# Optimization experiments

Hardware: AMD Instinct MI355X
Metric: run time of the kernel (lower is better)

Reference implementation:

```python
import jax, jax.numpy as jnp
import numpy as np

B, T, D = 16384, 3, 512   # batch, task_num, input_dim
G = T + 1                  # expert groups (idx 0 shared)
NE = 4                     # experts per group
H, E = 512, 256            # expert hidden, expert output dim (layers=[512,256])
GH = 256                   # gate hidden
TH, TO = 128, 64           # tower hidden / output dims


def setup_inputs() -> dict:
    key = jax.random.key(0)
    ks = jax.random.split(key, 14)
    s = 0.02
    return {
        "inputs": jax.random.normal(ks[0], (B, G, D), jnp.float32),
        # expert MLPs: [group, expert, ...]
        "expert_W1": jax.random.normal(ks[1], (G, NE, D, H), jnp.float32) * s,
        "expert_b1": jnp.zeros((G, NE, H), jnp.float32),
        "expert_W2": jax.random.normal(ks[2], (G, NE, H, E), jnp.float32) * s,
        "expert_b2": jnp.zeros((G, NE, E), jnp.float32),
        # per-task gates (softmax over G*NE experts)
        "gate_W1": jax.random.normal(ks[3], (T, D, GH), jnp.float32) * s,
        "gate_b1": jnp.zeros((T, GH), jnp.float32),
        "gate_W2": jax.random.normal(ks[4], (T, GH, G * NE), jnp.float32) * s,
        "gate_b2": jnp.zeros((T, G * NE), jnp.float32),
        # per-task towers (is_last=True)
        "tower_W1": jax.random.normal(ks[5], (T, E, TH), jnp.float32) * s,
        "tower_b1": jnp.zeros((T, TH), jnp.float32),
        "tower_W2": jax.random.normal(ks[6], (T, TH, TO), jnp.float32) * s,
        "tower_b2": jnp.zeros((T, TO), jnp.float32),
    }


def reference(inputs, expert_W1, expert_b1, expert_W2, expert_b2,
              gate_W1, gate_b1, gate_W2, gate_b2,
              tower_W1, tower_b1, tower_W2, tower_b2):
    b = inputs.shape[0]
    g, ne = expert_W1.shape[0], expert_W1.shape[1]
    t_num = gate_W1.shape[0]

    # All expert groups in one batched einsum: [B, G, NE, E]
    h1 = jax.nn.relu(jnp.einsum('bgd,gndh->bgnh', inputs, expert_W1) + expert_b1)
    emb = jnp.einsum('bgnh,gnhe->bgne', h1, expert_W2) + expert_b2

    # Task gates on (task input + shared input): softmax over G*NE experts
    gin = inputs[:, 1:, :] + inputs[:, :1, :]                      # [B, T, D]
    gh = jax.nn.relu(jnp.einsum('btd,tdh->bth', gin, gate_W1) + gate_b1)
    gw = jax.nn.softmax(jnp.einsum('bth,thk->btk', gh, gate_W2) + gate_b2, axis=-1)  # [B,T,G*NE]

    emb_sg = jax.lax.stop_gradient(emb)
    group_ids = jnp.arange(g)
    outs = []
    for t in range(t_num):
        # gradient flows only through shared group (0) and own group (t+1)
        keep = (group_ids == 0) | (group_ids == t + 1)              # [G]
        masked = jnp.where(keep[None, :, None, None], emb, emb_sg)  # [B,G,NE,E]
        agg = jnp.einsum('bk,bke->be', gw[:, t], masked.reshape(b, g * ne, -1))  # [B,E]
        th = jax.nn.relu(agg @ tower_W1[t] + tower_b1[t])
        outs.append(th @ tower_W2[t] + tower_b2[t])                 # [B,TO]
    return jnp.concatenate(outs, axis=1)                           # [B, T*TO]
```

## Files before the change

kernel.cpp:

```cpp
#include <hip/hip_runtime.h>
#include <math.h>

#define B_N  16384
#define T_N  3
#define D_N  512
#define G_N  4
#define NE_N 4
#define H_N  512
#define E_N  256
#define GH_N 256
#define K16  16
#define TH_N 128
#define TO_N 64

typedef __attribute__((ext_vector_type(8))) short short8;
typedef __attribute__((ext_vector_type(4))) float floatx4;

__device__ __forceinline__ unsigned short f2bf(float f) {
    union { float f; unsigned u; } v; v.f = f;
    unsigned r = (v.u + 0x7fffu + ((v.u >> 16) & 1u)) >> 16;
    return (unsigned short)r;
}
__device__ __forceinline__ float bf2f(unsigned short h) {
    union { unsigned u; float f; } v; v.u = ((unsigned)h) << 16;
    return v.f;
}
__device__ __forceinline__ unsigned pack2(float lo, float hi) {
    return ((unsigned)f2bf(hi) << 16) | (unsigned)f2bf(lo);
}

typedef const __attribute__((address_space(1))) void gvoid_t;
typedef __attribute__((address_space(3))) void lvoid_t;

#if __has_builtin(__builtin_amdgcn_global_load_lds)
#define HAVE_GLL 1
__device__ __forceinline__ void load_lds16(const void* g, void* l) {
    __builtin_amdgcn_global_load_lds((gvoid_t*)g, (lvoid_t*)l, 16, 0, 0);
}
#else
#define HAVE_GLL 0
#endif

__global__ __launch_bounds__(256) void convert_inputs(
    const float* __restrict__ x, unsigned short* __restrict__ xb,
    unsigned short* __restrict__ ginb)
{
    const long b = blockIdx.x;
    const int tid = threadIdx.x;
    const float* xr = x + b * (G_N * D_N);
    unsigned short* xo = xb + b * (G_N * D_N);
    unsigned short* go = ginb + b * (T_N * D_N);
    float2 v0 = *(const float2*)&xr[tid * 2];
    *(unsigned*)&xo[tid * 2] = pack2(v0.x, v0.y);
    #pragma unroll
    for (int g = 1; g < G_N; ++g) {
        float2 v = *(const float2*)&xr[g * D_N + tid * 2];
        *(unsigned*)&xo[g * D_N + tid * 2] = pack2(v.x, v.y);
        *(unsigned*)&go[(g - 1) * D_N + tid * 2] = pack2(v.x + v0.x, v.y + v0.y);
    }
}

__global__ __launch_bounds__(256) void prep_kernel(
    const float* __restrict__ eW1, const float* __restrict__ eW2,
    const float* __restrict__ gW1, const float* __restrict__ tW1,
    const float* __restrict__ tW2,
    unsigned short* __restrict__ W1t, unsigned short* __restrict__ W2t,
    unsigned short* __restrict__ G1t, unsigned short* __restrict__ TW1t,
    unsigned short* __restrict__ TW2t,
    const float* __restrict__ x, unsigned short* __restrict__ xb,
    unsigned short* __restrict__ ginb)
{
    const int bid = blockIdx.x;
    if (bid < 6648) {
        const float* in; unsigned short* out; int K, N, nx, local;
        if (bid < 4096)      { in = eW1; out = W1t;  K = 512; N = 512; nx = 16; local = bid; }
        else if (bid < 6144) { in = eW2; out = W2t;  K = 512; N = 256; nx = 8;  local = bid - 4096; }
        else if (bid < 6528) { in = gW1; out = G1t;  K = 512; N = 256; nx = 8;  local = bid - 6144; }
        else if (bid < 6624) { in = tW1; out = TW1t; K = 256; N = 128; nx = 4;  local = bid - 6528; }
        else                 { in = tW2; out = TW2t; K = 128; N = 64;  nx = 2;  local = bid - 6624; }
        const int ny = K / 32;
        const int xt = local % nx;
        const int yt = (local / nx) % ny;
        const int z  = local / (nx * ny);
        __shared__ float tile[32][33];
        const int tx = threadIdx.x & 31, ty = threadIdx.x >> 5;
        const long zo = (long)z * K * N;
        const int n0 = xt * 32, k0 = yt * 32;
        #pragma unroll
        for (int i = 0; i < 4; ++i)
            tile[ty + 8 * i][tx] = in[zo + (long)(k0 + ty + 8 * i) * N + n0 + tx];
        __syncthreads();
        #pragma unroll
        for (int i = 0; i < 4; ++i)
            out[zo + (long)(n0 + ty + 8 * i) * K + k0 + tx] = f2bf(tile[tx][ty + 8 * i]);
    } else {
        const long b = bid - 6648;
        const int tid = threadIdx.x;
        const float* xr = x + b * (G_N * D_N);
        unsigned short* xo = xb + b * (G_N * D_N);
        unsigned short* go = ginb + b * (T_N * D_N);
        float2 v0 = *(const float2*)&xr[tid * 2];
        *(unsigned*)&xo[tid * 2] = pack2(v0.x, v0.y);
        #pragma unroll
        for (int g = 1; g < G_N; ++g) {
            float2 v = *(const float2*)&xr[g * D_N + tid * 2];
            *(unsigned*)&xo[g * D_N + tid * 2] = pack2(v.x, v.y);
            *(unsigned*)&go[(g - 1) * D_N + tid * 2] = pack2(v.x + v0.x, v.y + v0.y);
        }
    }
}

template<int RELU>
__global__ __launch_bounds__(256) void gemm_bf16(
    const unsigned short* __restrict__ A, int lda, int a_zoff,
    const unsigned short* __restrict__ Bt, int bt_zoff,
    const float* __restrict__ bias, int bias_zoff,
    unsigned short* __restrict__ C, int ldc, int c_zoff, int K)
{
    __shared__ __align__(16) unsigned short As[2][128 * 32];
    __shared__ __align__(16) unsigned short Bs[2][128 * 32];
    const int tid = threadIdx.x;
    const int z = blockIdx.z;
    const long m0 = (long)blockIdx.x * 128;
    const long n0 = (long)blockIdx.y * 128;
    const unsigned short* Ab = A + (long)z * a_zoff + m0 * lda;
    const unsigned short* Bb = Bt + (long)z * bt_zoff + n0 * K;
    const int lane16 = tid & 15;
    const int quad = (tid & 63) >> 4;
    const int wave = tid >> 6;
    const int wm = (wave >> 1) * 64;
    const int wn = (wave & 1) * 64;
    const int srow = tid >> 2;
    const int scolsw = (((tid & 3) ^ ((tid >> 3) & 3)) * 8);
    const int cw8 = ((quad ^ ((lane16 >> 1) & 3)) * 8);

    floatx4 acc[4][4] = {};

    for (int k0 = 0; k0 < K; k0 += 64) {
        #pragma unroll
        for (int h = 0; h < 2; ++h) {
            const int kh = k0 + h * 32;
#if HAVE_GLL
            load_lds16(Ab + (long)srow * lda + kh + scolsw, &As[h][tid * 8]);
            load_lds16(Ab + (long)(srow + 64) * lda + kh + scolsw, &As[h][2048 + tid * 8]);
            load_lds16(Bb + (long)srow * K + kh + scolsw, &Bs[h][tid * 8]);
            load_lds16(Bb + (long)(srow + 64) * K + kh + scolsw, &Bs[h][2048 + tid * 8]);
#else
            *(uint4*)&As[h][tid * 8] = *(const uint4*)(Ab + (long)srow * lda + kh + scolsw);
            *(uint4*)&As[h][2048 + tid * 8] = *(const uint4*)(Ab + (long)(srow + 64) * lda + kh + scolsw);
            *(uint4*)&Bs[h][tid * 8] = *(const uint4*)(Bb + (long)srow * K + kh + scolsw);
            *(uint4*)&Bs[h][2048 + tid * 8] = *(const uint4*)(Bb + (long)(srow + 64) * K + kh + scolsw);
#endif
        }
        __syncthreads();
        #pragma unroll
        for (int h = 0; h < 2; ++h) {
            short8 a[4], b[4];
            #pragma unroll
            for (int mi = 0; mi < 4; ++mi)
                a[mi] = *(const short8*)&As[h][(wm + mi * 16 + lane16) * 32 + cw8];
            #pragma unroll
            for (int ni = 0; ni < 4; ++ni)
                b[ni] = *(const short8*)&Bs[h][(wn + ni * 16 + lane16) * 32 + cw8];
            #pragma unroll
            for (int mi = 0; mi < 4; ++mi)
                #pragma unroll
                for (int ni = 0; ni < 4; ++ni)
                    acc[mi][ni] = __builtin_amdgcn_mfma_f32_16x16x32_bf16(
                        a[mi], b[ni], acc[mi][ni], 0, 0, 0);
        }
        __syncthreads();
    }

    unsigned short* Cb = C + (long)z * c_zoff + m0 * ldc + n0;
    const float* bb = bias + (long)z * bias_zoff + n0;
    #pragma unroll
    for (int mi = 0; mi < 4; ++mi) {
        #pragma unroll
        for (int ni = 0; ni < 4; ++ni) {
            const int col = wn + ni * 16 + lane16;
            const float bv = bb[col];
            #pragma unroll
            for (int r = 0; r < 4; ++r) {
                const int row = wm + mi * 16 + quad * 4 + r;
                float v = acc[mi][ni][r] + bv;
                if (RELU) v = fmaxf(v, 0.0f);
                Cb[(long)row * ldc + col] = f2bf(v);
            }
        }
    }
}

__global__ __launch_bounds__(256, 2) void expert_fused(
    const unsigned short* __restrict__ xb,
    const unsigned short* __restrict__ W1t,
    const float* __restrict__ eb1,
    const unsigned short* __restrict__ W2t,
    const float* __restrict__ eb2,
    unsigned short* __restrict__ embb)
{
    __shared__ __align__(16) unsigned short sm[33792];
    unsigned short* As  = sm;
    unsigned short* Bs  = sm + 8192;
    unsigned short* h1s = sm + 16384;

    const int tid = threadIdx.x;
    const unsigned bid = blockIdx.x;
    const int e = ((bid & 7) << 1) | ((bid >> 3) & 1);
    const long m0 = (long)(bid >> 4) * 128;
    const int g = e >> 2;

    const unsigned short* Ab  = xb + m0 * 2048 + g * 512;
    const unsigned short* W1b = W1t + (long)e * (512 * 512);
    const unsigned short* W2b = W2t + (long)e * (256 * 512);

    const int lane16 = tid & 15;
    const int quad = (tid & 63) >> 4;
    const int wave = tid >> 6;
    const int wm  = (wave >> 1) * 64;
    const int wn  = (wave & 1) * 64;
    const int wn2 = (wave & 1) * 128;
    const int srow = tid >> 2;
    const int scolsw = (((tid & 3) ^ ((tid >> 3) & 3)) * 8);
    const int cw8 = ((quad ^ ((lane16 >> 1) & 3)) * 8);

    floatx4 acc2[4][8] = {};

    for (int nc = 0; nc < 4; ++nc) {
        const unsigned short* Bb = W1b + ((long)nc << 16);
        floatx4 acc[4][4] = {};
        for (int k0 = 0; k0 < 512; k0 += 64) {
            #pragma unroll
            for (int h = 0; h < 2; ++h) {
                const int kh = k0 + h * 32;
#if HAVE_GLL
                load_lds16(Ab + (long)srow * 2048 + kh + scolsw, &As[h * 4096 + tid * 8]);
                load_lds16(Ab + (long)(srow + 64) * 2048 + kh + scolsw, &As[h * 4096 + 2048 + tid * 8]);
                load_lds16(Bb + (long)srow * 512 + kh + scolsw, &Bs[h * 4096 + tid * 8]);
                load_lds16(Bb + (long)(srow + 64) * 512 + kh + scolsw, &Bs[h * 4096 + 2048 + tid * 8]);
#else
                *(uint4*)&As[h * 4096 + tid * 8] = *(const uint4*)(Ab + (long)srow * 2048 + kh + scolsw);
                *(uint4*)&As[h * 4096 + 2048 + tid * 8] = *(const uint4*)(Ab + (long)(srow + 64) * 2048 + kh + scolsw);
                *(uint4*)&Bs[h * 4096 + tid * 8] = *(const uint4*)(Bb + (long)srow * 512 + kh + scolsw);
                *(uint4*)&Bs[h * 4096 + 2048 + tid * 8] = *(const uint4*)(Bb + (long)(srow + 64) * 512 + kh + scolsw);
#endif
            }
            __syncthreads();
            #pragma unroll
            for (int h = 0; h < 2; ++h) {
                short8 b[4];
                #pragma unroll
                for (int ni = 0; ni < 4; ++ni)
                    b[ni] = *(const short8*)&Bs[h * 4096 + (wn + ni * 16 + lane16) * 32 + cw8];
                #pragma unroll
                for (int mi = 0; mi < 4; ++mi) {
                    short8 a = *(const short8*)&As[h * 4096 + (wm + mi * 16 + lane16) * 32 + cw8];
                    #pragma unroll
                    for (int ni = 0; ni < 4; ++ni)
                        acc[mi][ni] = __builtin_amdgcn_mfma_f32_16x16x32_bf16(
                            a, b[ni], acc[mi][ni], 0, 0, 0);
                }
            }
            __syncthreads();
        }
        #pragma unroll
        for (int mi = 0; mi < 4; ++mi) {
            #pragma unroll
            for (int ni = 0; ni < 4; ++ni) {
                const int col = wn + ni * 16 + lane16;
                const float bv = eb1[e * 512 + nc * 128 + col];
                #pragma unroll
                for (int r = 0; r < 4; ++r) {
                    const int row = wm + mi * 16 + quad * 4 + r;
                    h1s[row * 136 + col] = f2bf(fmaxf(acc[mi][ni][r] + bv, 0.0f));
                }
            }
        }
        __syncthreads();
        #pragma unroll
        for (int ks = 0; ks < 128; ks += 32) {
            #pragma unroll
            for (int i = 0; i < 4; ++i) {
#if HAVE_GLL
                load_lds16(W2b + (long)(srow + 64 * i) * 512 + nc * 128 + ks + scolsw,
                           &As[i * 2048 + tid * 8]);
#else
                *(uint4*)&As[i * 2048 + tid * 8] =
                    *(const uint4*)(W2b + (long)(srow + 64 * i) * 512 + nc * 128 + ks + scolsw);
#endif
            }
            __syncthreads();
            #pragma unroll
            for (int nh = 0; nh < 2; ++nh) {
                short8 b2[4];
                #pragma unroll
                for (int nj = 0; nj < 4; ++nj)
                    b2[nj] = *(const short8*)&As[(wn2 + nh * 64 + nj * 16 + lane16) * 32 + cw8];
                #pragma unroll
                for (int mi = 0; mi < 4; ++mi) {
                    short8 a2 = *(const short8*)&h1s[(wm + mi * 16 + lane16) * 136 + ks + quad * 8];
                    #pragma unroll
                    for (int nj = 0; nj < 4; ++nj)
                        acc2[mi][nh * 4 + nj] = __builtin_amdgcn_mfma_f32_16x16x32_bf16(
                            a2, b2[nj], acc2[mi][nh * 4 + nj], 0, 0, 0);
                }
            }
            __syncthreads();
        }
    }

    unsigned short* Cb = embb + m0 * 4096 + (long)e * 256;
    #pragma unroll
    for (int mi = 0; mi < 4; ++mi) {
        #pragma unroll
        for (int j = 0; j < 8; ++j) {
            const int col = wn2 + (j >> 2) * 64 + (j & 3) * 16 + lane16;
            const float bv = eb2[e * 256 + col];
            #pragma unroll
            for (int r = 0; r < 4; ++r) {
                const int row = wm + mi * 16 + quad * 4 + r;
                Cb[(long)row * 4096 + col] = f2bf(acc2[mi][j][r] + bv);
            }
        }
    }
}

__global__ __launch_bounds__(256) void gate2_softmax(
    const unsigned short* __restrict__ gh, const float* __restrict__ W2,
    const float* __restrict__ b2, float* __restrict__ gw)
{
    const int t = blockIdx.y;
    const long b0 = (long)blockIdx.x * 64;
    const int tid = threadIdx.x;
    __shared__ __align__(16) unsigned short ghs[64 * 256];
    __shared__ float ls[64 * 16];
    #pragma unroll
    for (int it = 0; it < 8; ++it) {
        int seg = it * 256 + tid;
        int row = seg >> 5;
        int col = (seg & 31) * 8;
        *(uint4*)&ghs[seg * 8] =
            *(const uint4*)&gh[(b0 + row) * (T_N * GH_N) + (long)t * GH_N + col];
    }
    __syncthreads();
    const float* W2t = W2 + (long)t * GH_N * K16;
    #pragma unroll
    for (int it = 0; it < 4; ++it) {
        int o = it * 256 + tid;
        int b = o >> 4, k = o & 15;
        float acc = b2[t * K16 + k];
        #pragma unroll 8
        for (int h = 0; h < GH_N; ++h)
            acc += bf2f(ghs[b * 256 + h]) * W2t[h * K16 + k];
        ls[o] = acc;
    }
    __syncthreads();
    if (tid < 64) {
        float m = -1e30f;
        #pragma unroll
        for (int k = 0; k < 16; ++k) m = fmaxf(m, ls[tid * 16 + k]);
        float e[16], s = 0.f;
        #pragma unroll
        for (int k = 0; k < 16; ++k) { e[k] = expf(ls[tid * 16 + k] - m); s += e[k]; }
        const float inv = 1.0f / s;
        float* gwp = gw + (b0 + tid) * (T_N * K16) + (long)t * K16;
        #pragma unroll
        for (int k = 0; k < 16; ++k) gwp[k] = e[k] * inv;
    }
}

__global__ __launch_bounds__(256) void agg_kernel(
    const unsigned short* __restrict__ emb, const float* __restrict__ gw,
    unsigned short* __restrict__ aggb, long bc)
{
    const long b = (long)blockIdx.x * 8 + (threadIdx.x >> 5);
    const int e0 = (threadIdx.x & 31) * 8;
    const unsigned short* er = emb + b * 4096 + e0;
    const float* gwr = gw + b * 48;
    float a0[8] = {}, a1[8] = {}, a2[8] = {};
    #pragma unroll
    for (int k = 0; k < 16; ++k) {
        short8 v = *(const short8*)(er + (long)k * 256);
        const float w0 = gwr[k], w1 = gwr[16 + k], w2 = gwr[32 + k];
        #pragma unroll
        for (int j = 0; j < 8; ++j) {
            float f = bf2f((unsigned short)v[j]);
            a0[j] += w0 * f; a1[j] += w1 * f; a2[j] += w2 * f;
        }
    }
    unsigned r0[4] = {pack2(a0[0], a0[1]), pack2(a0[2], a0[3]),
                      pack2(a0[4], a0[5]), pack2(a0[6], a0[7])};
    unsigned r1[4] = {pack2(a1[0], a1[1]), pack2(a1[2], a1[3]),
                      pack2(a1[4], a1[5]), pack2(a1[6], a1[7])};
    unsigned r2[4] = {pack2(a2[0], a2[1]), pack2(a2[2], a2[3]),
                      pack2(a2[4], a2[5]), pack2(a2[6], a2[7])};
    *(uint4*)(aggb + 0L * bc * 256 + b * 256 + e0) = *(uint4*)r0;
    *(uint4*)(aggb + 1L * bc * 256 + b * 256 + e0) = *(uint4*)r1;
    *(uint4*)(aggb + 2L * bc * 256 + b * 256 + e0) = *(uint4*)r2;
}

__global__ __launch_bounds__(256) void tower_fused(
    const unsigned short* __restrict__ aggb, long bc,
    const unsigned short* __restrict__ w1t, const float* __restrict__ tb1,
    const unsigned short* __restrict__ w2t, const float* __restrict__ tb2,
    float* __restrict__ out)
{
    __shared__ __align__(16) unsigned short sm[26112];
    unsigned short* As  = sm;
    unsigned short* Bs  = sm + 4096;
    unsigned short* th  = sm;
    unsigned short* w2s = sm + 17408;
    const int tid = threadIdx.x;
    const int t = blockIdx.y;
    const long m0 = (long)blockIdx.x * 128;
    const unsigned short* Ab = aggb + (long)t * bc * 256 + m0 * 256;
    const unsigned short* Bb = w1t + (long)t * (TH_N * E_N);
    const int lane16 = tid & 15;
    const int quad = (tid & 63) >> 4;
    const int wave = tid >> 6;
    const int wm = (wave >> 1) * 64;
    const int wn = (wave & 1) * 64;
    const int srow = tid >> 2;
    const int scolsw = (((tid & 3) ^ ((tid >> 3) & 3)) * 8);
    const int cw8 = ((quad ^ ((lane16 >> 1) & 3)) * 8);

    #pragma unroll
    for (int i = 0; i < 4; ++i) {
        const int seg = i * 256 + tid;
        const int row = seg >> 4, cb = (seg & 15) * 8;
        *(uint4*)&w2s[row * 136 + cb] =
            *(const uint4*)&w2t[(long)t * (TO_N * TH_N) + (long)row * 128 + cb];
    }

    floatx4 acc[4][4] = {};
    for (int k0 = 0; k0 < 256; k0 += 32) {
#if HAVE_GLL
        load_lds16(Ab + (long)srow * 256 + k0 + scolsw, &As[tid * 8]);
        load_lds16(Ab + (long)(srow + 64) * 256 + k0 + scolsw, &As[2048 + tid * 8]);
        load_lds16(Bb + (long)srow * 256 + k0 + scolsw, &Bs[tid * 8]);
        load_lds16(Bb + (long)(srow + 64) * 256 + k0 + scolsw, &Bs[2048 + tid * 8]);
#else
        *(uint4*)&As[tid * 8] = *(const uint4*)(Ab + (long)srow * 256 + k0 + scolsw);
        *(uint4*)&As[2048 + tid * 8] = *(const uint4*)(Ab + (long)(srow + 64) * 256 + k0 + scolsw);
        *(uint4*)&Bs[tid * 8] = *(const uint4*)(Bb + (long)srow * 256 + k0 + scolsw);
        *(uint4*)&Bs[2048 + tid * 8] = *(const uint4*)(Bb + (long)(srow + 64) * 256 + k0 + scolsw);
#endif
        __syncthreads();
        short8 a[4], b[4];
        #pragma unroll
        for (int mi = 0; mi < 4; ++mi)
            a[mi] = *(const short8*)&As[(wm + mi * 16 + lane16) * 32 + cw8];
        #pragma unroll
        for (int ni = 0; ni < 4; ++ni)
            b[ni] = *(const short8*)&Bs[(wn + ni * 16 + lane16) * 32 + cw8];
        #pragma unroll
        for (int mi = 0; mi < 4; ++mi)
            #pragma unroll
            for (int ni = 0; ni < 4; ++ni)
                acc[mi][ni] = __builtin_amdgcn_mfma_f32_16x16x32_bf16(
                    a[mi], b[ni], acc[mi][ni], 0, 0, 0);
        __syncthreads();
    }

    #pragma unroll
    for (int mi = 0; mi < 4; ++mi) {
        #pragma unroll
        for (int ni = 0; ni < 4; ++ni) {
            const int col = wn + ni * 16 + lane16;
            const float bv = tb1[t * TH_N + col];
            #pragma unroll
            for (int r = 0; r < 4; ++r) {
                const int row = wm + mi * 16 + quad * 4 + r;
                th[row * 136 + col] = f2bf(fmaxf(acc[mi][ni][r] + bv, 0.0f));
            }
        }
    }
    __syncthreads();

    floatx4 acc2[2][4] = {};
    #pragma unroll
    for (int kk = 0; kk < 4; ++kk) {
        short8 a2[2], b2[4];
        #pragma unroll
        for (int mi = 0; mi < 2; ++mi)
            a2[mi] = *(const short8*)&th[(wave * 32 + mi * 16 + lane16) * 136 + kk * 32 + quad * 8];
        #pragma unroll
        for (int ni = 0; ni < 4; ++ni)
            b2[ni] = *(const short8*)&w2s[(ni * 16 + lane16) * 136 + kk * 32 + quad * 8];
        #pragma unroll
        for (int mi = 0; mi < 2; ++mi)
            #pragma unroll
            for (int ni = 0; ni < 4; ++ni)
                acc2[mi][ni] = __builtin_amdgcn_mfma_f32_16x16x32_bf16(
                    a2[mi], b2[ni], acc2[mi][ni], 0, 0, 0);
    }
    #pragma unroll
    for (int mi = 0; mi < 2; ++mi) {
        #pragma unroll
        for (int ni = 0; ni < 4; ++ni) {
            const int col = ni * 16 + lane16;
            const float bv = tb2[t * TO_N + col];
            #pragma unroll
            for (int r = 0; r < 4; ++r) {
                const int row = wave * 32 + mi * 16 + quad * 4 + r;
                out[(m0 + row) * (T_N * TO_N) + t * TO_N + col] = acc2[mi][ni][r] + bv;
            }
        }
    }
}

extern "C" void kernel_launch(void* const* d_in, const int* in_sizes, int n_in,
                              void* d_out, int out_size, void* d_ws, size_t ws_size,
                              hipStream_t stream)
{
    const float* x   = (const float*)d_in[0];
    const float* eW1 = (const float*)d_in[1];
    const float* eb1 = (const float*)d_in[2];
    const float* eW2 = (const float*)d_in[3];
    const float* eb2 = (const float*)d_in[4];
    const float* gW1 = (const float*)d_in[5];
    const float* gb1 = (const float*)d_in[6];
    const float* gW2 = (const float*)d_in[7];
    const float* gb2 = (const float*)d_in[8];
    const float* tW1 = (const float*)d_in[9];
    const float* tb1 = (const float*)d_in[10];
    const float* tW2 = (const float*)d_in[11];
    const float* tb2 = (const float*)d_in[12];
    float* out = (float*)d_out;

    char* ws = (char*)d_ws;
    unsigned short* W1t  = (unsigned short*)(ws + 0);
    unsigned short* W2t  = (unsigned short*)(ws + 8388608);
    unsigned short* G1t  = (unsigned short*)(ws + 12582912);
    unsigned short* TW1t = (unsigned short*)(ws + 13369344);
    unsigned short* TW2t = (unsigned short*)(ws + 13565952);
    const size_t WFIX = 13615104;

    long BCo = 0;
    for (long co = 16384; co >= 128; co >>= 1)
        if (WFIX + (size_t)co * 18624 <= ws_size) { BCo = co; break; }
    if (BCo == 0) return;

    char* p = ws + WFIX;
    unsigned short* xb   = (unsigned short*)p; p += BCo * 4096;
    unsigned short* ginb = (unsigned short*)p; p += BCo * 3072;
    unsigned short* embb = (unsigned short*)p; p += BCo * 8192;
    unsigned short* gh   = (unsigned short*)p; p += BCo * 1536;
    float*          gw   = (float*)p;          p += BCo * 192;
    unsigned short* aggb = (unsigned short*)p;

    const long n_o = B_N / BCo;

    const long nconv = (n_o == 1) ? BCo : 0;
    prep_kernel<<<dim3((unsigned)(6648 + nconv)), 256, 0, stream>>>(
        eW1, eW2, gW1, tW1, tW2, W1t, W2t, G1t, TW1t, TW2t, x, xb, ginb);

    for (long c = 0; c < n_o; ++c) {
        const float* xc = x + c * BCo * (G_N * D_N);
        float* outc = out + c * BCo * (T_N * TO_N);

        if (n_o > 1)
            convert_inputs<<<BCo, 256, 0, stream>>>(xc, xb, ginb);
        gemm_bf16<1><<<dim3(BCo / 128, 2, 3), 256, 0, stream>>>(
            ginb, 1536, 512, G1t, 131072, gb1, 256, gh, 768, 256, 512);
        gate2_softmax<<<dim3(BCo / 64, 3), 256, 0, stream>>>(gh, gW2, gb2, gw);
        expert_fused<<<dim3((BCo / 128) * 16), 256, 0, stream>>>(
            xb, W1t, eb1, W2t, eb2, embb);
        agg_kernel<<<BCo / 8, 256, 0, stream>>>(embb, gw, aggb, BCo);
        tower_fused<<<dim3(BCo / 128, 3), 256, 0, stream>>>(
            aggb, BCo, TW1t, tb1, TW2t, tb2, outc);
    }
}
```

Baseline: 593.1 us.

## Fuse gate GEMM, second gate layer and softmax into one MFMA kernel

Replaces the generic gate hidden-layer GEMM plus the scalar gate2_softmax kernel with a single gate_fused kernel. The 128x256 ReLU hidden tile stays in swizzled LDS, and the second gate layer runs on MFMA with bf16-converted weights. Softmax is done with cross-lane shuffles, which removes the gh round-trip through global memory, one launch, and the scalar FMA loop. In exchange the kernel drops double-buffered K staging, has fewer blocks (one per 128 rows per task), and rounds W2 to bf16.

Result: faster. 563.0 us (median of 2 runs) (-5.1%).

```diff
diff --git a/kernel.cpp b/kernel.cpp
--- a/kernel.cpp
+++ b/kernel.cpp
@@ -110,83 +110,118 @@
     }
 }
 
-template<int RELU>
-__global__ __launch_bounds__(256) void gemm_bf16(
-    const unsigned short* __restrict__ A, int lda, int a_zoff,
-    const unsigned short* __restrict__ Bt, int bt_zoff,
-    const float* __restrict__ bias, int bias_zoff,
-    unsigned short* __restrict__ C, int ldc, int c_zoff, int K)
-{
-    __shared__ __align__(16) unsigned short As[2][128 * 32];
-    __shared__ __align__(16) unsigned short Bs[2][128 * 32];
+__global__ __launch_bounds__(256) void gate_fused(
+    const unsigned short* __restrict__ ginb,
+    const unsigned short* __restrict__ G1t,
+    const float* __restrict__ gb1,
+    const float* __restrict__ gW2,
+    const float* __restrict__ gb2,
+    float* __restrict__ gw)
+{
+    __shared__ __align__(16) unsigned short sm[40960];
+    unsigned short* As  = sm;
+    unsigned short* Bs  = sm + 4096;
+    unsigned short* w2s = sm;
+    unsigned short* ghs = sm + 8192;
+
     const int tid = threadIdx.x;
-    const int z = blockIdx.z;
-    const long m0 = (long)blockIdx.x * 128;
-    const long n0 = (long)blockIdx.y * 128;
-    const unsigned short* Ab = A + (long)z * a_zoff + m0 * lda;
-    const unsigned short* Bb = Bt + (long)z * bt_zoff + n0 * K;
+    const int t = blockIdx.y;
+    const long b0 = (long)blockIdx.x * 128;
+    const unsigned short* Ab = ginb + b0 * 1536 + (long)t * 512;
+
     const int lane16 = tid & 15;
     const int quad = (tid & 63) >> 4;
     const int wave = tid >> 6;
     const int wm = (wave >> 1) * 64;
     const int wn = (wave & 1) * 64;
     const int srow = tid >> 2;
-    const int scolsw = (((tid & 3) ^ ((tid >> 3) & 3)) * 8);
+    const int scol = (((tid & 3) ^ ((tid >> 3) & 3)) * 8);
     const int cw8 = ((quad ^ ((lane16 >> 1) & 3)) * 8);
 
-    floatx4 acc[4][4] = {};
-
-    for (int k0 = 0; k0 < K; k0 += 64) {
-        #pragma unroll
-        for (int h = 0; h < 2; ++h) {
-            const int kh = k0 + h * 32;
+    #pragma unroll
+    for (int ncc = 0; ncc < 2; ++ncc) {
+        const unsigned short* Bb = G1t + (long)t * 131072 + (long)(ncc * 128) * 512;
+        floatx4 acc[4][4] = {};
+        for (int k0 = 0; k0 < 512; k0 += 32) {
 #if HAVE_GLL
-            load_lds16(Ab + (long)srow * lda + kh + scolsw, &As[h][tid * 8]);
-            load_lds16(Ab + (long)(srow + 64) * lda + kh + scolsw, &As[h][2048 + tid * 8]);
-            load_lds16(Bb + (long)srow * K + kh + scolsw, &Bs[h][tid * 8]);
-            load_lds16(Bb + (long)(srow + 64) * K + kh + scolsw, &Bs[h][2048 + tid * 8]);
+            load_lds16(Ab + (long)srow * 1536 + k0 + scol, &As[tid * 8]);
+            load_lds16(Ab + (long)(srow + 64) * 1536 + k0 + scol, &As[2048 + tid * 8]);
+            load_lds16(Bb + (long)srow * 512 + k0 + scol, &Bs[tid * 8]);
+            load_lds16(Bb + (long)(srow + 64) * 512 + k0 + scol, &Bs[2048 + tid * 8]);
 #else
-            *(uint4*)&As[h][tid * 8] = *(const uint4*)(Ab + (long)srow * lda + kh + scolsw);
-            *(uint4*)&As[h][2048 + tid * 8] = *(const uint4*)(Ab + (long)(srow + 64) * lda + kh + scolsw);
-            *(uint4*)&Bs[h][tid * 8] = *(const uint4*)(Bb + (long)srow * K + kh + scolsw);
-            *(uint4*)&Bs[h][2048 + tid * 8] = *(const uint4*)(Bb + (long)(srow + 64) * K + kh + scolsw);
+            *(uint4*)&As[tid * 8] = *(const uint4*)(Ab + (long)srow * 1536 + k0 + scol);
+            *(uint4*)&As[2048 + tid * 8] = *(const uint4*)(Ab + (long)(srow + 64) * 1536 + k0 + scol);
+            *(uint4*)&Bs[tid * 8] = *(const uint4*)(Bb + (long)srow * 512 + k0 + scol);
+            *(uint4*)&Bs[2048 + tid * 8] = *(const uint4*)(Bb + (long)(srow + 64) * 512 + k0 + scol);
 #endif
-        }
-        __syncthreads();
-        #pragma unroll
-        for (int h = 0; h < 2; ++h) {
+            __syncthreads();
             short8 a[4], b[4];
             #pragma unroll
             for (int mi = 0; mi < 4; ++mi)
-                a[mi] = *(const short8*)&As[h][(wm + mi * 16 + lane16) * 32 + cw8];
+                a[mi] = *(const short8*)&As[(wm + mi * 16 + lane16) * 32 + cw8];
             #pragma unroll
             for (int ni = 0; ni < 4; ++ni)
-                b[ni] = *(const short8*)&Bs[h][(wn + ni * 16 + lane16) * 32 + cw8];
+                b[ni] = *(const short8*)&Bs[(wn + ni * 16 + lane16) * 32 + cw8];
             #pragma unroll
             for (int mi = 0; mi < 4; ++mi)
                 #pragma unroll
                 for (int ni = 0; ni < 4; ++ni)
                     acc[mi][ni] = __builtin_amdgcn_mfma_f32_16x16x32_bf16(
                         a[mi], b[ni], acc[mi][ni], 0, 0, 0);
-        }
-        __syncthreads();
-    }
-
-    unsigned short* Cb = C + (long)z * c_zoff + m0 * ldc + n0;
-    const float* bb = bias + (long)z * bias_zoff + n0;
-    #pragma unroll
-    for (int mi = 0; mi < 4; ++mi) {
-        #pragma unroll
-        for (int ni = 0; ni < 4; ++ni) {
-            const int col = wn + ni * 16 + lane16;
-            const float bv = bb[col];
-            #pragma unroll
-            for (int r = 0; r < 4; ++r) {
-                const int row = wm + mi * 16 + quad * 4 + r;
-                float v = acc[mi][ni][r] + bv;
-                if (RELU) v = fmaxf(v, 0.0f);
-                Cb[(long)row * ldc + col] = f2bf(v);
-            }
+            __syncthreads();
+        }
+        #pragma unroll
+        for (int mi = 0; mi < 4; ++mi) {
+            #pragma unroll
+            for (int ni = 0; ni < 4; ++ni) {
+                const int col = ncc * 128 + wn + ni * 16 + lane16;
+                const float bv = gb1[t * GH_N + col];
+                #pragma unroll
+                for (int r = 0; r < 4; ++r) {
+                    const int row = wm + mi * 16 + quad * 4 + r;
+                    const int pc = (col & 7) | ((((col >> 3) ^ (row & 7))) << 3);
+                    ghs[row * 256 + pc] = f2bf(fmaxf(acc[mi][ni][r] + bv, 0.0f));
+                }
+            }
+        }
+    }
+    {
+        const float* W2p = gW2 + (long)t * (GH_N * K16);
+        #pragma unroll
+        for (int j = 0; j < 16; ++j)
+            w2s[j * 264 + tid] = f2bf(W2p[(long)tid * K16 + j]);
+    }
+    __syncthreads();
+
+    floatx4 ag[2] = {};
+    #pragma unroll
+    for (int kk = 0; kk < 8; ++kk) {
+        short8 bfr = *(const short8*)&w2s[lane16 * 264 + kk * 32 + quad * 8];
+        #pragma unroll
+        for (int mi = 0; mi < 2; ++mi) {
+            const int row = wave * 32 + mi * 16 + lane16;
+            short8 afr = *(const short8*)&ghs[row * 256 + (((kk * 4 + quad) ^ (row & 7)) << 3)];
+            ag[mi] = __builtin_amdgcn_mfma_f32_16x16x32_bf16(afr, bfr, ag[mi], 0, 0, 0);
+        }
+    }
+
+    const float bb2 = gb2[t * K16 + lane16];
+    #pragma unroll
+    for (int mi = 0; mi < 2; ++mi) {
+        float v[4], m = -1e30f;
+        #pragma unroll
+        for (int r = 0; r < 4; ++r) { v[r] = ag[mi][r] + bb2; }
+        #pragma unroll
+        for (int r = 0; r < 4; ++r) {
+            float mv = v[r];
+            #pragma unroll
+            for (int d = 1; d < 16; d <<= 1) mv = fmaxf(mv, __shfl_xor(mv, d));
+            float e = expf(v[r] - mv);
+            float s = e;
+            #pragma unroll
+            for (int d = 1; d < 16; d <<= 1) s += __shfl_xor(s, d);
+            const int row = wave * 32 + mi * 16 + quad * 4 + r;
+            gw[(b0 + row) * (T_N * K16) + (long)t * K16 + lane16] = e / s;
         }
     }
 }
@@ -322,50 +357,6 @@
                 Cb[(long)row * 4096 + col] = f2bf(acc2[mi][j][r] + bv);
             }
         }
-    }
-}
-
-__global__ __launch_bounds__(256) void gate2_softmax(
-    const unsigned short* __restrict__ gh, const float* __restrict__ W2,
-    const float* __restrict__ b2, float* __restrict__ gw)
-{
-    const int t = blockIdx.y;
-    const long b0 = (long)blockIdx.x * 64;
-    const int tid = threadIdx.x;
-    __shared__ __align__(16) unsigned short ghs[64 * 256];
-    __shared__ float ls[64 * 16];
-    #pragma unroll
-    for (int it = 0; it < 8; ++it) {
-        int seg = it * 256 + tid;
-        int row = seg >> 5;
-        int col = (seg & 31) * 8;
-        *(uint4*)&ghs[seg * 8] =
-            *(const uint4*)&gh[(b0 + row) * (T_N * GH_N) + (long)t * GH_N + col];
-    }
-    __syncthreads();
-    const float* W2t = W2 + (long)t * GH_N * K16;
-    #pragma unroll
-    for (int it = 0; it < 4; ++it) {
-        int o = it * 256 + tid;
-        int b = o >> 4, k = o & 15;
-        float acc = b2[t * K16 + k];
-        #pragma unroll 8
-        for (int h = 0; h < GH_N; ++h)
-            acc += bf2f(ghs[b * 256 + h]) * W2t[h * K16 + k];
-        ls[o] = acc;
-    }
-    __syncthreads();
-    if (tid < 64) {
-        float m = -1e30f;
-        #pragma unroll
-        for (int k = 0; k < 16; ++k) m = fmaxf(m, ls[tid * 16 + k]);
-        float e[16], s = 0.f;
-        #pragma unroll
-        for (int k = 0; k < 16; ++k) { e[k] = expf(ls[tid * 16 + k] - m); s += e[k]; }
-        const float inv = 1.0f / s;
-        float* gwp = gw + (b0 + tid) * (T_N * K16) + (long)t * K16;
-        #pragma unroll
-        for (int k = 0; k < 16; ++k) gwp[k] = e[k] * inv;
     }
 }
 
@@ -548,6 +539,7 @@
     unsigned short* gh   = (unsigned short*)p; p += BCo * 1536;
     float*          gw   = (float*)p;          p += BCo * 192;
     unsigned short* aggb = (unsigned short*)p;
+    (void)gh;
 
     const long n_o = B_N / BCo;
 
@@ -561,9 +553,8 @@
 
         if (n_o > 1)
             convert_inputs<<<BCo, 256, 0, stream>>>(xc, xb, ginb);
-        gemm_bf16<1><<<dim3(BCo / 128, 2, 3), 256, 0, stream>>>(
-            ginb, 1536, 512, G1t, 131072, gb1, 256, gh, 768, 256, 512);
-        gate2_softmax<<<dim3(BCo / 64, 3), 256, 0, stream>>>(gh, gW2, gb2, gw);
+        gate_fused<<<dim3(BCo / 128, 3), 256, 0, stream>>>(
+            ginb, G1t, gb1, gW2, gb2, gw);
         expert_fused<<<dim3((BCo / 128) * 16), 256, 0, stream>>>(
             xb, W1t, eb1, W2t, eb2, embb);
         agg_kernel<<<BCo / 8, 256, 0, stream>>>(embb, gw, aggb, BCo);
```
